# Optimization experiments

Hardware: AMD Instinct MI355X
Metric: run time of the kernel (lower is better)

The kernel has to match this reference:

```python
import jax, jax.numpy as jnp
import numpy as np

B, G, H = 16, 1708, 5


def setup_inputs() -> dict:
    key = jax.random.key(0)
    k0, k1, k2, k3 = jax.random.split(key, 4)
    x = jax.random.normal(k0, (B, G), dtype=jnp.float32)
    # xavier_normal on (H, G, 1): std = gain*sqrt(2/(fan_in+fan_out)) ~ gain*sqrt(2/G)
    std_qk = 5.0 * np.sqrt(2.0 / (G + 1))   # gain=5 for WQ, WK
    std_v = 1.0 * np.sqrt(2.0 / (G + 1))    # gain=1 for WV
    WQ = jax.random.normal(k1, (H, G, 1), dtype=jnp.float32) * std_qk
    WK = jax.random.normal(k2, (H, G, 1), dtype=jnp.float32) * std_qk
    WV = jax.random.normal(k3, (H, G, 1), dtype=jnp.float32) * std_v
    W0 = jnp.ones((H,), dtype=jnp.float32)  # torch.Tensor(n_head*[1])
    return {"x": x, "WQ": WQ, "WK": WK, "WV": WV, "W0": W0}


def reference(x, WQ, WK, WV, W0):
    # x: (B, G); WQ/WK/WV: (H, G, 1); W0: (H,)
    g = x.shape[1]
    off_diag = 1.0 - jnp.eye(g, dtype=x.dtype)  # mask applied AFTER softmax
    head_outs = []
    for h in range(WQ.shape[0]):  # small fixed head loop keeps peak memory low
        q = x * WQ[h, :, 0]  # (B, G)
        k = x * WK[h, :, 0]  # (B, G)
        v = x * WV[h, :, 0]  # (B, G)
        # scores[b,i,j] = q[b,i] * k[b,j]  (broadcast outer product, not dot-product)
        scores = q[:, :, None] * k[:, None, :]  # (B, G, G)
        z = jax.nn.softmax(scores, axis=2) * off_diag
        head_outs.append(jnp.einsum('bij,bj->bi', z, v))  # (B, G)
    out_seq = jnp.stack(head_outs, axis=-1)  # (B, G, H)
    return jnp.einsum('bgh,h->bg', out_seq, W0)  # (B, G)
```

## Files before the change

### kernel.cpp

```cpp
#include <hip/hip_runtime.h>

constexpr int B = 16;
constexpr int G = 1708;
constexpr int H = 5;
constexpr int TPB = 256;
constexpr int M1 = 17;

#define LOG2E 1.4426950408889634f


__device__ float g_mom[B * H * 2 * M1];

__device__ __forceinline__ float fast_exp(float x) {
#if __has_builtin(__builtin_amdgcn_exp2f)
    return __builtin_amdgcn_exp2f(x * LOG2E);
#else
    return __expf(x);
#endif
}

__constant__ float INVFACT[M1] = {
    (float)(1.0),                    (float)(1.0),
    (float)(1.0 / 2.0),              (float)(1.0 / 6.0),
    (float)(1.0 / 24.0),             (float)(1.0 / 120.0),
    (float)(1.0 / 720.0),            (float)(1.0 / 5040.0),
    (float)(1.0 / 40320.0),          (float)(1.0 / 362880.0),
    (float)(1.0 / 3628800.0),        (float)(1.0 / 39916800.0),
    (float)(1.0 / 479001600.0),      (float)(1.0 / 6227020800.0),
    (float)(1.0 / 87178291200.0),    (float)(1.0 / 1307674368000.0),
    (float)(1.0 / 20922789888000.0)
};

__global__ __launch_bounds__(TPB)
void moments_kernel(const float* __restrict__ x,
                    const float* __restrict__ WK,
                    const float* __restrict__ WV)
{
    const int h = blockIdx.x % H;
    const int b = blockIdx.x / H;
    const float* __restrict__ xb = x  + b * G;
    const float* __restrict__ wk = WK + h * G;
    const float* __restrict__ wv = WV + h * G;

    float S[M1], T[M1];
#pragma unroll
    for (int m = 0; m < M1; ++m) { S[m] = 0.f; T[m] = 0.f; }

    for (int j = threadIdx.x; j < G; j += TPB) {
        const float xj = xb[j];
        const float k  = xj * wk[j];
        const float v  = xj * wv[j];
        float pw = 1.f;
#pragma unroll
        for (int m = 0; m < M1; ++m) {
            S[m] += pw;
            T[m] = fmaf(v, pw, T[m]);
            pw *= k;
        }
    }

#pragma unroll
    for (int m = 0; m < M1; ++m) {
#pragma unroll
        for (int off = 32; off >= 1; off >>= 1) {
            S[m] += __shfl_xor(S[m], off, 64);
            T[m] += __shfl_xor(T[m], off, 64);
        }
    }

    __shared__ float red[2][4][M1];
    const int wave = threadIdx.x >> 6;
    const int lane = threadIdx.x & 63;
    if (lane == 0) {
#pragma unroll
        for (int m = 0; m < M1; ++m) {
            red[0][wave][m] = S[m];
            red[1][wave][m] = T[m];
        }
    }
    __syncthreads();

    if (threadIdx.x < 2 * M1) {
        const int which = threadIdx.x / M1;
        const int m     = threadIdx.x % M1;
        const float s = (red[which][0][m] + red[which][1][m]) +
                        (red[which][2][m] + red[which][3][m]);
        g_mom[(b * H + h) * (2 * M1) + which * M1 + m] = s * INVFACT[m];
    }
}

__global__ __launch_bounds__(TPB)
void eval_kernel(const float* __restrict__ x,
                 const float* __restrict__ WQ,
                 const float* __restrict__ WK,
                 const float* __restrict__ WV,
                 const float* __restrict__ W0,
                 float* __restrict__ out)
{
    const int b = blockIdx.y;
    const int i = blockIdx.x * TPB + threadIdx.x;
    if (i >= G) return;

    const float xi = x[b * G + i];
    float acc = 0.f;

#pragma unroll
    for (int h = 0; h < H; ++h) {
        const float* __restrict__ mp = g_mom + (b * H + h) * (2 * M1);
        const float q = xi * WQ[h * G + i];

        float D = mp[M1 - 1];
        float N = mp[2 * M1 - 1];
#pragma unroll
        for (int m = M1 - 2; m >= 0; --m) {
            D = fmaf(D, q, mp[m]);
            N = fmaf(N, q, mp[M1 + m]);
        }

        const float k   = xi * WK[h * G + i];
        const float v   = xi * WV[h * G + i];
        const float eii = fast_exp(q * k);
        acc = fmaf(W0[h], (N - eii * v) / D, acc);
    }
    out[b * G + i] = acc;
}

extern "C" void kernel_launch(void* const* d_in, const int* in_sizes, int n_in,
                              void* d_out, int out_size, void* d_ws, size_t ws_size,
                              hipStream_t stream) {
    const float* x  = (const float*)d_in[0];
    const float* WQ = (const float*)d_in[1];
    const float* WK = (const float*)d_in[2];
    const float* WV = (const float*)d_in[3];
    const float* W0 = (const float*)d_in[4];
    float* out = (float*)d_out;

    moments_kernel<<<B * H, TPB, 0, stream>>>(x, WK, WV);

    dim3 grid2((G + TPB - 1) / TPB, B);
    eval_kernel<<<grid2, TPB, 0, stream>>>(x, WQ, WK, WV, W0, out);
}
```

Measured before the change: 69.76 us.

## Split moment reduction across G slices with atomics and shrink eval blocks

The moments kernel now splits the G dimension into 4 slices per (batch, head), launching 4x more blocks and combining partial sums with atomicAdd into a workspace buffer zeroed by a memset. Power computation uses four interleaved chains stepping by k^4 to shorten the dependency chain, and the shuffle reduction stops at 8 lanes with a wider shared-memory reduction. The eval kernel uses 64-thread blocks for more blocks across CUs. This adds a memset launch and atomics, and the final sums become order-nondeterministic.

```diff
diff --git a/kernel.cpp b/kernel.cpp
--- a/kernel.cpp
+++ b/kernel.cpp
@@ -3,13 +3,14 @@
 constexpr int B = 16;
 constexpr int G = 1708;
 constexpr int H = 5;
-constexpr int TPB = 256;
 constexpr int M1 = 17;
+constexpr int JS = 4;
+constexpr int JPS = G / JS;
+constexpr int TPB1 = 256;
+constexpr int TPB2 = 64;
 
 #define LOG2E 1.4426950408889634f
 
-
-__device__ float g_mom[B * H * 2 * M1];
 
 __device__ __forceinline__ float fast_exp(float x) {
 #if __has_builtin(__builtin_amdgcn_exp2f)
@@ -31,13 +32,17 @@
     (float)(1.0 / 20922789888000.0)
 };
 
-__global__ __launch_bounds__(TPB)
+__global__ __launch_bounds__(TPB1)
 void moments_kernel(const float* __restrict__ x,
                     const float* __restrict__ WK,
-                    const float* __restrict__ WV)
+                    const float* __restrict__ WV,
+                    float* __restrict__ g_mom)
 {
-    const int h = blockIdx.x % H;
-    const int b = blockIdx.x / H;
+    const int slice = blockIdx.x % JS;
+    const int h     = (blockIdx.x / JS) % H;
+    const int b     = blockIdx.x / (JS * H);
+    const int j0    = slice * JPS;
+
     const float* __restrict__ xb = x  + b * G;
     const float* __restrict__ wk = WK + h * G;
     const float* __restrict__ wv = WV + h * G;
@@ -46,59 +51,73 @@
 #pragma unroll
     for (int m = 0; m < M1; ++m) { S[m] = 0.f; T[m] = 0.f; }
 
-    for (int j = threadIdx.x; j < G; j += TPB) {
+    for (int t = threadIdx.x; t < JPS; t += TPB1) {
+        const int j   = j0 + t;
         const float xj = xb[j];
         const float k  = xj * wk[j];
         const float v  = xj * wv[j];
-        float pw = 1.f;
+        const float k2 = k * k;
+        const float k4 = k2 * k2;
+        float p0 = 1.f, p1 = k, p2 = k2, p3 = k2 * k;
 #pragma unroll
-        for (int m = 0; m < M1; ++m) {
-            S[m] += pw;
-            T[m] = fmaf(v, pw, T[m]);
-            pw *= k;
+        for (int gblk = 0; gblk < 4; ++gblk) {
+            const int base = gblk * 4;
+            S[base + 0] += p0; T[base + 0] = fmaf(v, p0, T[base + 0]); p0 *= k4;
+            S[base + 1] += p1; T[base + 1] = fmaf(v, p1, T[base + 1]); p1 *= k4;
+            S[base + 2] += p2; T[base + 2] = fmaf(v, p2, T[base + 2]); p2 *= k4;
+            S[base + 3] += p3; T[base + 3] = fmaf(v, p3, T[base + 3]); p3 *= k4;
         }
+        S[16] += p0; T[16] = fmaf(v, p0, T[16]);
     }
 
 #pragma unroll
     for (int m = 0; m < M1; ++m) {
 #pragma unroll
-        for (int off = 32; off >= 1; off >>= 1) {
+        for (int off = 8; off <= 32; off <<= 1) {
             S[m] += __shfl_xor(S[m], off, 64);
             T[m] += __shfl_xor(T[m], off, 64);
         }
     }
 
-    __shared__ float red[2][4][M1];
+    __shared__ float red[4 * 8][2 * M1];
     const int wave = threadIdx.x >> 6;
     const int lane = threadIdx.x & 63;
-    if (lane == 0) {
+    if (lane < 8) {
+        const int row = wave * 8 + lane;
 #pragma unroll
         for (int m = 0; m < M1; ++m) {
-            red[0][wave][m] = S[m];
-            red[1][wave][m] = T[m];
+            red[row][m]      = S[m];
+            red[row][M1 + m] = T[m];
         }
     }
     __syncthreads();
 
     if (threadIdx.x < 2 * M1) {
-        const int which = threadIdx.x / M1;
-        const int m     = threadIdx.x % M1;
-        const float s = (red[which][0][m] + red[which][1][m]) +
-                        (red[which][2][m] + red[which][3][m]);
-        g_mom[(b * H + h) * (2 * M1) + which * M1 + m] = s * INVFACT[m];
+        const int m = threadIdx.x % M1;
+        float s0 = 0.f, s1 = 0.f, s2 = 0.f, s3 = 0.f;
+#pragma unroll
+        for (int r = 0; r < 32; r += 4) {
+            s0 += red[r + 0][threadIdx.x];
+            s1 += red[r + 1][threadIdx.x];
+            s2 += red[r + 2][threadIdx.x];
+            s3 += red[r + 3][threadIdx.x];
+        }
+        const float s = ((s0 + s1) + (s2 + s3)) * INVFACT[m];
+        atomicAdd(&g_mom[(b * H + h) * (2 * M1) + threadIdx.x], s);
     }
 }
 
-__global__ __launch_bounds__(TPB)
+__global__ __launch_bounds__(TPB2)
 void eval_kernel(const float* __restrict__ x,
                  const float* __restrict__ WQ,
                  const float* __restrict__ WK,
                  const float* __restrict__ WV,
                  const float* __restrict__ W0,
+                 const float* __restrict__ g_mom,
                  float* __restrict__ out)
 {
     const int b = blockIdx.y;
-    const int i = blockIdx.x * TPB + threadIdx.x;
+    const int i = blockIdx.x * TPB2 + threadIdx.x;
     if (i >= G) return;
 
     const float xi = x[b * G + i];
@@ -133,10 +152,13 @@
     const float* WK = (const float*)d_in[2];
     const float* WV = (const float*)d_in[3];
     const float* W0 = (const float*)d_in[4];
-    float* out = (float*)d_out;
+    float* out   = (float*)d_out;
+    float* g_mom = (float*)d_ws;
 
-    moments_kernel<<<B * H, TPB, 0, stream>>>(x, WK, WV);
+    hipMemsetAsync(g_mom, 0, (size_t)(B * H * 2 * M1) * sizeof(float), stream);
 
-    dim3 grid2((G + TPB - 1) / TPB, B);
-    eval_kernel<<<grid2, TPB, 0, stream>>>(x, WQ, WK, WV, W0, out);
+    moments_kernel<<<B * H * JS, TPB1, 0, stream>>>(x, WK, WV, g_mom);
+
+    dim3 grid2((G + TPB2 - 1) / TPB2, B);
+    eval_kernel<<<grid2, TPB2, 0, stream>>>(x, WQ, WK, WV, W0, g_mom, out);
 }
```

After: 69.60 us. Within noise of the previous version (-0.2%).
